# Kernel optimization log

Measured on AMD Instinct MI355X. Metric: run time of the kernel, lower is better.

## Reference

```python
import jax, jax.numpy as jnp
import numpy as np

NUM_GRAPHS = 64


def setup_inputs() -> dict:
    key = jax.random.key(0)
    ks = jax.random.split(key, 8)
    N, E, D_IN, D_H = 50000, 800000, 128, 256
    x = jax.random.uniform(ks[0], (N, D_IN), dtype=jnp.float32)
    edge_index = jax.random.randint(ks[1], (2, E), 0, N, dtype=jnp.int64)
    batch = jnp.sort(jax.random.randint(ks[2], (N,), 0, NUM_GRAPHS, dtype=jnp.int64))
    s = 1.0 / np.sqrt(D_IN)
    s2 = 1.0 / np.sqrt(D_H)
    W1_rel = jax.random.normal(ks[3], (D_IN, D_H), dtype=jnp.float32) * s
    W1_root = jax.random.normal(ks[4], (D_IN, D_H), dtype=jnp.float32) * s
    b1 = jnp.zeros((D_H,), jnp.float32)
    W2_rel = jax.random.normal(ks[5], (D_H, D_H), dtype=jnp.float32) * s2
    W2_root = jax.random.normal(ks[6], (D_H, D_H), dtype=jnp.float32) * s2
    b2 = jnp.zeros((D_H,), jnp.float32)
    return {"x": x, "edge_index": edge_index, "batch": batch,
            "W1_rel": W1_rel, "W1_root": W1_root, "b1": b1,
            "W2_rel": W2_rel, "W2_root": W2_root, "b2": b2}


def reference(x, edge_index, batch, W1_rel, W1_root, b1, W2_rel, W2_root, b2):
    N = x.shape[0]
    src, dst = edge_index[0], edge_index[1]

    # handcrafted features: per-label fraction of total feature mass + log(graph_size)
    graph_size = jnp.sum(x)
    handcrafted = jnp.concatenate([jnp.sum(x, axis=0) / graph_size,
                                   jnp.log(graph_size)[None]])

    def graph_conv(h, W_rel, W_root, b):
        # PyG GraphConv (aggr='add'): out_i = W_rel @ sum_{j->i} h_j + W_root @ h_i + b
        agg = jax.ops.segment_sum(h[src], dst, num_segments=N)  # [N, d]
        return agg @ W_rel + h @ W_root + b

    h = jax.nn.relu(graph_conv(x, W1_rel, W1_root, b1))
    # layers 2..num_layers share the same weights (module instance reused in original)
    for _ in range(2):
        h = jax.nn.relu(graph_conv(h, W2_rel, W2_root, b2))

    # global_mean_pool over batch ids
    counts = jax.ops.segment_sum(jnp.ones((N,), h.dtype), batch, num_segments=NUM_GRAPHS)
    pooled = jax.ops.segment_sum(h, batch, num_segments=NUM_GRAPHS)
    pooled = pooled / jnp.maximum(counts, 1.0)[:, None]
    return pooled, handcrafted
```

## Files before the change

kernel.cpp:

```cpp
#include <hip/hip_runtime.h>
#include <hip/hip_bf16.h>
#include <string.h>

#define NN 50000
#define NE 800000
#define DIN 128
#define DH 256
#define NG 64
#define PSPLIT 32
#define GCAP 2048

typedef short bf16x8 __attribute__((ext_vector_type(8)));
typedef float f32x4 __attribute__((ext_vector_type(4)));
typedef unsigned int u32x2 __attribute__((ext_vector_type(2)));

__device__ __forceinline__ float bf2f(__hip_bfloat16 v) { return __bfloat162float(v); }
__device__ __forceinline__ float bfbits(unsigned int lo16) {
  unsigned int u = lo16 << 16;
  float f;
  memcpy(&f, &u, 4);
  return f;
}
__device__ __forceinline__ unsigned int packbf2(float x, float y) {
  __hip_bfloat16 bx = __float2bfloat16(x), by = __float2bfloat16(y);
  unsigned short ux, uy;
  memcpy(&ux, &bx, 2);
  memcpy(&uy, &by, 2);
  return (unsigned int)ux | ((unsigned int)uy << 16);
}

__device__ __forceinline__ float loadF(const void* p, long i, int fbf) {
  return fbf ? bf2f(((const __hip_bfloat16*)p)[i]) : ((const float*)p)[i];
}
__device__ __forceinline__ void storeF(void* p, long i, float v, int fbf) {
  if (fbf) ((__hip_bfloat16*)p)[i] = __float2bfloat16(v);
  else ((float*)p)[i] = v;
}
__device__ __forceinline__ int loadI(const void* p, long i, int i64) {
  return i64 ? (int)((const long long*)p)[i] : ((const int*)p)[i];
}

__global__ void k_zero_detect(int* __restrict__ p, int n, const void* __restrict__ x,
                              const void* __restrict__ ei, int* __restrict__ flags) {
  int i = blockIdx.x * blockDim.x + threadIdx.x;
  int stride = gridDim.x * blockDim.x;
  for (int k = i; k < n; k += stride) p[k] = 0;
  if (blockIdx.x == 0) {
    __shared__ int s_f32sig, s_i32sig;
    if (threadIdx.x == 0) { s_f32sig = 0; s_i32sig = 0; }
    __syncthreads();
    int t = threadIdx.x;
    const unsigned short* u = (const unsigned short*)x;
    int f = 0;
    for (int j = 2 * t; j < 8192; j += 512) if (u[j] >= 0x4000) f = 1;
    const unsigned int* w = (const unsigned int*)ei;
    int g = 0;
    for (int j = 2 * t + 1; j < 8192; j += 512) if (w[j] != 0u) g = 1;
    if (f) atomicOr(&s_f32sig, 1);
    if (g) atomicOr(&s_i32sig, 1);
    __syncthreads();
    if (t == 0) { flags[0] = s_f32sig ? 0 : 1; flags[1] = s_i32sig ? 0 : 1; }
  }
}

__global__ __launch_bounds__(256) void k_prep(
    const void* __restrict__ x, __hip_bfloat16* __restrict__ xs,
    float* __restrict__ colsum, const int* __restrict__ flags) {
  int fbf = flags[0];
  int t = threadIdx.x;
  int lane16 = t & 15;
  int rowoff = t >> 4;
  float acc[8] = {};
  for (int r = blockIdx.x * 16 + rowoff; r < NN; r += gridDim.x * 16) {
    uint4 o;
    if (fbf) {
      uint4 v = ((const uint4*)x)[(long)r * 16 + lane16];
      acc[0] += bfbits(v.x & 0xffffu); acc[1] += bfbits(v.x >> 16);
      acc[2] += bfbits(v.y & 0xffffu); acc[3] += bfbits(v.y >> 16);
      acc[4] += bfbits(v.z & 0xffffu); acc[5] += bfbits(v.z >> 16);
      acc[6] += bfbits(v.w & 0xffffu); acc[7] += bfbits(v.w >> 16);
      o = v;
    } else {
      float4 a = ((const float4*)x)[(long)r * 32 + lane16 * 2];
      float4 b = ((const float4*)x)[(long)r * 32 + lane16 * 2 + 1];
      acc[0] += a.x; acc[1] += a.y; acc[2] += a.z; acc[3] += a.w;
      acc[4] += b.x; acc[5] += b.y; acc[6] += b.z; acc[7] += b.w;
      o.x = packbf2(a.x, a.y); o.y = packbf2(a.z, a.w);
      o.z = packbf2(b.x, b.y); o.w = packbf2(b.z, b.w);
    }
    ((uint4*)xs)[((long)(lane16 >> 2) * NN + r) * 4 + (lane16 & 3)] = o;
  }
  __shared__ float s[16][DIN];
#pragma unroll
  for (int k = 0; k < 8; ++k) s[rowoff][lane16 * 8 + k] = acc[k];
  __syncthreads();
  if (t < DIN) {
    float v = 0.f;
#pragma unroll
    for (int ro = 0; ro < 16; ++ro) v += s[ro][t];
    atomicAdd(&colsum[t], v);
  }
}

__global__ void k_handcrafted(const float* __restrict__ colsum, void* __restrict__ out,
                              const int* __restrict__ flags) {
  __shared__ float s[DIN];
  int fbf = flags[0];
  int t = threadIdx.x;
  s[t] = colsum[t];
  __syncthreads();
  for (int off = DIN / 2; off > 0; off >>= 1) {
    if (t < off) s[t] += s[t + off];
    __syncthreads();
  }
  float g = s[0];
  storeF(out, NG * DH + t, colsum[t] / g, fbf);
  if (t == 0) storeF(out, NG * DH + DIN, logf(g), fbf);
}

__global__ void k_pack_w(const void* __restrict__ Wrel, const void* __restrict__ Wroot,
                         const void* __restrict__ bias, __hip_bfloat16* __restrict__ pack,
                         float* __restrict__ biasf, const int* __restrict__ flags, int K) {
  int fbf = flags[0];
  int KS = K >> 5;
  int total = 2 * K * DH;
  int i = blockIdx.x * blockDim.x + threadIdx.x;
  int stride = gridDim.x * blockDim.x;
  for (int p = i; p < total; p += stride) {
    int m = p / (K * DH);
    int r = p % (K * DH);
    int j = r & 7;
    int l = (r >> 3) & 63;
    int q2 = r >> 9;
    int ks = q2 % KS;
    int ct = q2 / KS;
    int kk = ks * 32 + (l >> 4) * 8 + j;
    int col = ct * 16 + (l & 15);
    const void* W = m ? Wroot : Wrel;
    pack[p] = __float2bfloat16(loadF(W, (long)kk * DH + col, fbf));
  }
  if (i < DH) biasf[i] = loadF(bias, i, fbf);
}

__global__ void k_deg(const void* __restrict__ ei, int* __restrict__ cnt,
                      const int* __restrict__ flags) {
  int i64 = flags[1];
  int e = blockIdx.x * blockDim.x + threadIdx.x;
  int stride = gridDim.x * blockDim.x;
  for (; e < NE; e += stride) {
    int d = loadI(ei, (long)NE + e, i64);
    d = min(max(d, 0), NN - 1);
    atomicAdd(&cnt[d], 1);
  }
}

#define SCAN_B 256
__global__ void k_scan1(const int* __restrict__ cnt, int* __restrict__ rowptr,
                        int* __restrict__ bsum) {
  __shared__ int s[SCAN_B];
  int b = blockIdx.x, t = threadIdx.x;
  int i = b * SCAN_B + t;
  int v = (i < NN) ? cnt[i] : 0;
  s[t] = v;
  __syncthreads();
  for (int off = 1; off < SCAN_B; off <<= 1) {
    int xv = (t >= off) ? s[t - off] : 0;
    __syncthreads();
    s[t] += xv;
    __syncthreads();
  }
  if (i < NN) rowptr[i] = s[t] - v;
  if (t == SCAN_B - 1) bsum[b] = s[t];
}

__global__ void k_scan2(int* __restrict__ bsum, int nb) {
  __shared__ int s[SCAN_B];
  int t = threadIdx.x;
  int v = (t < nb) ? bsum[t] : 0;
  s[t] = v;
  __syncthreads();
  for (int off = 1; off < SCAN_B; off <<= 1) {
    int xv = (t >= off) ? s[t - off] : 0;
    __syncthreads();
    s[t] += xv;
    __syncthreads();
  }
  if (t < nb) bsum[t] = s[t] - v;
}

__global__ void k_scan3b(int* __restrict__ rowptr, const int* __restrict__ bsum,
                         const void* __restrict__ batch, int* __restrict__ gstart,
                         int* __restrict__ gend, const int* __restrict__ flags) {
  int i64 = flags[1];
  int i = blockIdx.x * blockDim.x + threadIdx.x;
  int stride = gridDim.x * blockDim.x;
  for (; i < NN; i += stride) {
    rowptr[i] += bsum[i >> 8];
    int b = min(max(loadI(batch, i, i64), 0), NG - 1);
    int bp = (i == 0) ? -1 : min(max(loadI(batch, i - 1, i64), 0), NG - 1);
    if (b != bp) gstart[b] = i;
    int bn = (i == NN - 1) ? -1 : min(max(loadI(batch, i + 1, i64), 0), NG - 1);
    if (b != bn) gend[b] = i + 1;
  }
  if (blockIdx.x == 0 && threadIdx.x == 0) rowptr[NN] = NE;
}

__global__ void k_fill(const void* __restrict__ ei, const int* __restrict__ rowptr,
                       int* __restrict__ cur, int* __restrict__ srcs,
                       const int* __restrict__ flags) {
  int i64 = flags[1];
  int e = blockIdx.x * blockDim.x + threadIdx.x;
  int stride = gridDim.x * blockDim.x;
  for (; e < NE; e += stride) {
    int s = loadI(ei, e, i64);
    int d = loadI(ei, (long)NE + e, i64);
    s = min(max(s, 0), NN - 1);
    d = min(max(d, 0), NN - 1);
    int p = atomicAdd(&cur[d], 1);
    srcs[rowptr[d] + p] = s;
  }
}

template <int K>
__global__ __launch_bounds__(256) void k_gathers(
    const int* __restrict__ rowptr, const int* __restrict__ srcs,
    const __hip_bfloat16* __restrict__ hs, __hip_bfloat16* __restrict__ agg) {
  constexpr int SL = K / 32;
  constexpr int HALVES = 8 / SL;
  constexpr int NPH = (NN + HALVES - 1) / HALVES;
  constexpr int NPB = 16;
  __shared__ int se[GCAP];
  __shared__ int sb[2];
  int role = blockIdx.x & 7;
  int nb = blockIdx.x >> 3;
  int s = role / HALVES;
  int half = role % HALVES;
  int t = threadIdx.x;
  int n0 = half * NPH + nb * NPB;
  int nlim = min((half + 1) * NPH, NN);
  if (t == 0) {
    sb[0] = rowptr[min(n0, nlim)];
    sb[1] = rowptr[min(n0 + NPB, nlim)];
  }
  __syncthreads();
  int wbeg = sb[0];
  int wlen = min(sb[1] - wbeg, GCAP);
  for (int i = t; i < wlen; i += 256)
    se[i] = __builtin_nontemporal_load(&srcs[wbeg + i]);
  __syncthreads();
  int nsub = t >> 4;
  int sub = (t >> 3) & 1;
  int c = t & 7;
  int node = n0 + nsub;
  if (node >= nlim) return;
  const u32x2* hb = (const u32x2*)hs + (long)s * NN * 8 + c;
  u32x2* agg2 = (u32x2*)agg;
  int beg = rowptr[node], end = rowptr[node + 1];
  float a0 = 0.f, a1 = 0.f, a2 = 0.f, a3 = 0.f;
  if (end - wbeg <= wlen) {
    int ib = beg - wbeg, ie = end - wbeg;
    for (int i = ib + sub * 8; i < ie; i += 16) {
      int idx[8];
      float m[8];
      u32x2 v[8];
#pragma unroll
      for (int u = 0; u < 8; ++u) {
        int j = i + u;
        int ok = j < ie;
        idx[u] = se[ok ? j : ib];
        m[u] = ok ? 1.f : 0.f;
      }
#pragma unroll
      for (int u = 0; u < 8; ++u) v[u] = hb[(long)idx[u] * 8];
#pragma unroll
      for (int u = 0; u < 8; ++u) {
        a0 = fmaf(m[u], bfbits(v[u].x & 0xffffu), a0);
        a1 = fmaf(m[u], bfbits(v[u].x >> 16), a1);
        a2 = fmaf(m[u], bfbits(v[u].y & 0xffffu), a2);
        a3 = fmaf(m[u], bfbits(v[u].y >> 16), a3);
      }
    }
  } else {
    for (int i = beg + sub * 8; i < end; i += 16) {
      int idx[8];
      float m[8];
      u32x2 v[8];
#pragma unroll
      for (int u = 0; u < 8; ++u) {
        int j = i + u;
        int ok = j < end;
        idx[u] = __builtin_nontemporal_load(&srcs[ok ? j : beg]);
        m[u] = ok ? 1.f : 0.f;
      }
#pragma unroll
      for (int u = 0; u < 8; ++u) v[u] = hb[(long)idx[u] * 8];
#pragma unroll
      for (int u = 0; u < 8; ++u) {
        a0 = fmaf(m[u], bfbits(v[u].x & 0xffffu), a0);
        a1 = fmaf(m[u], bfbits(v[u].x >> 16), a1);
        a2 = fmaf(m[u], bfbits(v[u].y & 0xffffu), a2);
        a3 = fmaf(m[u], bfbits(v[u].y >> 16), a3);
      }
    }
  }
  a0 += __shfl_xor(a0, 8);
  a1 += __shfl_xor(a1, 8);
  a2 += __shfl_xor(a2, 8);
  a3 += __shfl_xor(a3, 8);
  if (sub == 0) {
    u32x2 o;
    o.x = packbf2(a0, a1);
    o.y = packbf2(a2, a3);
    __builtin_nontemporal_store(o, &agg2[(long)node * (K / 4) + s * 8 + c]);
  }
}

template <int K, bool OUTS>
__global__ __launch_bounds__(256, 4) void k_gemm(
    const __hip_bfloat16* __restrict__ A1, const __hip_bfloat16* __restrict__ A2,
    const __hip_bfloat16* __restrict__ Wpack, const float* __restrict__ bias,
    __hip_bfloat16* __restrict__ out) {
  constexpr int KS = K >> 5;
  int lane = threadIdx.x & 63;
  int wave = threadIdx.x >> 6;
  int m15 = lane & 15;
  int q = lane >> 4;
  int row0 = blockIdx.x * 32;
  const short* A1s = (const short*)A1;
  const short* A2s = (const short*)A2;
  const short* Wp = (const short*)Wpack;
  const int wrootOfs = K * DH;
  f32x4 acc[2][4] = {};
#pragma unroll
  for (int ks = 0; ks < KS; ++ks) {
    int kofs = ks * 32 + q * 8;
    bf16x8 a1[2], a2[2], b1[4], b2[4];
#pragma unroll
    for (int mt = 0; mt < 2; ++mt) {
      int r = row0 + mt * 16 + m15;
      if (r > NN - 1) r = NN - 1;
      a1[mt] = *(const bf16x8*)(A1s + (long)r * K + kofs);
      a2[mt] = *(const bf16x8*)(A2s + ((long)ks * NN + r) * 32 + q * 8);
    }
#pragma unroll
    for (int ct = 0; ct < 4; ++ct) {
      int gct = wave * 4 + ct;
      const short* base = Wp + ((gct * KS + ks) * 64 + lane) * 8;
      b1[ct] = *(const bf16x8*)(base);
      b2[ct] = *(const bf16x8*)(base + wrootOfs);
    }
#pragma unroll
    for (int mt = 0; mt < 2; ++mt)
#pragma unroll
      for (int ct = 0; ct < 4; ++ct) {
        acc[mt][ct] = __builtin_amdgcn_mfma_f32_16x16x32_bf16(a1[mt], b1[ct], acc[mt][ct], 0, 0, 0);
        acc[mt][ct] = __builtin_amdgcn_mfma_f32_16x16x32_bf16(a2[mt], b2[ct], acc[mt][ct], 0, 0, 0);
      }
  }
#pragma unroll
  for (int mt = 0; mt < 2; ++mt)
#pragma unroll
    for (int ct = 0; ct < 4; ++ct) {
      int col = (wave * 4 + ct) * 16 + m15;
      float bv = bias[col];
#pragma unroll
      for (int r = 0; r < 4; ++r) {
        int row = row0 + mt * 16 + q * 4 + r;
        if (row < NN) {
          float v = acc[mt][ct][r] + bv;
          long oidx = OUTS ? (((long)(col >> 5) * NN + row) * 32 + (col & 31))
                           : ((long)row * DH + col);
          out[oidx] = __float2bfloat16(fmaxf(v, 0.f));
        }
      }
    }
}

__global__ void k_poolpart(const int* __restrict__ gstart, const int* __restrict__ gend,
                           const __hip_bfloat16* __restrict__ h, float* __restrict__ pooled) {
  int g = blockIdx.x;
  int p = blockIdx.y;
  int j = threadIdx.x;
  int s = gstart[g], e = gend[g];
  int len = e - s;
  if (len <= 0) return;
  int chunk = (len + PSPLIT - 1) / PSPLIT;
  int rs = s + p * chunk;
  int re = min(rs + chunk, e);
  if (rs >= re) return;
  const unsigned int* h2 = (const unsigned int*)h;
  float a0 = 0.f, a1 = 0.f;
  for (int r = rs; r < re; ++r) {
    unsigned int v = h2[(long)r * 128 + j];
    a0 += bfbits(v & 0xffffu);
    a1 += bfbits(v >> 16);
  }
  atomicAdd(&pooled[g * DH + 2 * j], a0);
  atomicAdd(&pooled[g * DH + 2 * j + 1], a1);
}

__global__ void k_poolfin(const int* __restrict__ gstart, const int* __restrict__ gend,
                          const float* __restrict__ pooled, void* __restrict__ out,
                          const int* __restrict__ flags) {
  int fbf = flags[0];
  int g = blockIdx.x;
  int j = threadIdx.x;
  float cnt = fmaxf((float)(gend[g] - gstart[g]), 1.0f);
  storeF(out, (long)g * DH + j, pooled[g * DH + j] / cnt, fbf);
}

extern "C" void kernel_launch(void* const* d_in, const int* in_sizes, int n_in,
                              void* d_out, int out_size, void* d_ws, size_t ws_size,
                              hipStream_t stream) {
  const void* x = d_in[0];
  const void* ei = d_in[1];
  const void* batch = d_in[2];
  const void* W1r = d_in[3];
  const void* W1o = d_in[4];
  const void* b1 = d_in[5];
  const void* W2r = d_in[6];
  const void* W2o = d_in[7];
  const void* b2 = d_in[8];
  void* out = d_out;

  char* w = (char*)d_ws;
  auto alloc = [&](size_t bytes) -> char* {
    char* p = w;
    w += (bytes + 255) & ~(size_t)255;
    return p;
  };
  int* flags = (int*)alloc(64);
  const int zero_n = NN + NN + DIN + NG + NG + NG * DH;
  int* zreg = (int*)alloc((size_t)zero_n * 4);
  int* cnt = zreg;
  int* cur = cnt + NN;
  float* colsum = (float*)(cur + NN);
  int* gstart = (int*)(colsum + DIN);
  int* gend = gstart + NG;
  float* pooled = (float*)(gend + NG);
  int* rowptr = (int*)alloc((NN + 1) * 4);
  int* bsum = (int*)alloc(SCAN_B * 4);
  int* srcs = (int*)alloc((size_t)NE * 4);
  __hip_bfloat16* xs = (__hip_bfloat16*)alloc((size_t)NN * DIN * 2);
  __hip_bfloat16* aggb = (__hip_bfloat16*)alloc((size_t)NN * DH * 2);
  __hip_bfloat16* h1s = (__hip_bfloat16*)alloc((size_t)NN * DH * 2);
  __hip_bfloat16* h2s = (__hip_bfloat16*)alloc((size_t)NN * DH * 2);
  __hip_bfloat16* wp1 = (__hip_bfloat16*)alloc((size_t)2 * DIN * DH * 2);
  __hip_bfloat16* wp2 = (__hip_bfloat16*)alloc((size_t)2 * DH * DH * 2);
  float* b1f = (float*)alloc(DH * 4);
  float* b2f = (float*)alloc(DH * 4);
  __hip_bfloat16* hA = h1s;

  const int nblk = (NN + SCAN_B - 1) / SCAN_B;
  const int gemm_grid = (NN + 31) / 32;
  const int g256_grid = 8 * ((NN + 15) / 16);
  const int g128_grid = 8 * ((NN / 2 + 15) / 16);

  k_zero_detect<<<512, 256, 0, stream>>>(zreg, zero_n, x, ei, flags);

  k_pack_w<<<64, 256, 0, stream>>>(W1r, W1o, b1, wp1, b1f, flags, DIN);
  k_pack_w<<<128, 256, 0, stream>>>(W2r, W2o, b2, wp2, b2f, flags, DH);
  k_prep<<<1024, 256, 0, stream>>>(x, xs, colsum, flags);
  k_handcrafted<<<1, 128, 0, stream>>>(colsum, out, flags);

  k_deg<<<1024, 256, 0, stream>>>(ei, cnt, flags);
  k_scan1<<<nblk, SCAN_B, 0, stream>>>(cnt, rowptr, bsum);
  k_scan2<<<1, SCAN_B, 0, stream>>>(bsum, nblk);
  k_scan3b<<<256, 256, 0, stream>>>(rowptr, bsum, batch, gstart, gend, flags);
  k_fill<<<1024, 256, 0, stream>>>(ei, rowptr, cur, srcs, flags);

  k_gathers<DIN><<<g128_grid, 256, 0, stream>>>(rowptr, srcs, xs, aggb);
  k_gemm<DIN, true><<<gemm_grid, 256, 0, stream>>>(aggb, xs, wp1, b1f, h1s);
  k_gathers<DH><<<g256_grid, 256, 0, stream>>>(rowptr, srcs, h1s, aggb);
  k_gemm<DH, true><<<gemm_grid, 256, 0, stream>>>(aggb, h1s, wp2, b2f, h2s);
  k_gathers<DH><<<g256_grid, 256, 0, stream>>>(rowptr, srcs, h2s, aggb);
  k_gemm<DH, false><<<gemm_grid, 256, 0, stream>>>(aggb, h2s, wp2, b2f, hA);

  k_poolpart<<<dim3(NG, PSPLIT), 128, 0, stream>>>(gstart, gend, hA, pooled);
  k_poolfin<<<NG, DH, 0, stream>>>(gstart, gend, pooled, out, flags);
}
```

Baseline: 532.5 us.

## Balance gather work by splitting block edge ranges evenly across thread groups

Rewrites the CSR gather kernel so each block covers 32 nodes and splits its whole edge range evenly among 32 thread groups, instead of giving each node's edges to a fixed 16-thread group. Each edge is tagged with its local node via a binary search over row pointers, and partial sums are flushed into a shared-memory accumulator with LDS atomics whenever the node changes. This targets load imbalance from varying node degrees and raises per-thread memory-level parallelism with 16 loads in flight. In exchange it adds LDS atomics, a per-edge binary search, and padded shared accumulators.

```diff
diff --git a/kernel.cpp b/kernel.cpp
--- a/kernel.cpp
+++ b/kernel.cpp
@@ -8,7 +8,7 @@
 #define DH 256
 #define NG 64
 #define PSPLIT 32
-#define GCAP 2048
+#define GCAP 1024
 
 typedef short bf16x8 __attribute__((ext_vector_type(8)));
 typedef float f32x4 __attribute__((ext_vector_type(4)));
@@ -228,9 +228,10 @@
   constexpr int SL = K / 32;
   constexpr int HALVES = 8 / SL;
   constexpr int NPH = (NN + HALVES - 1) / HALVES;
-  constexpr int NPB = 16;
-  __shared__ int se[GCAP];
-  __shared__ int sb[2];
+  constexpr int NPB = 32;
+  __shared__ int srow[NPB + 1];
+  __shared__ unsigned int se[GCAP];
+  __shared__ float sacc[NPB * 33];
   int role = blockIdx.x & 7;
   int nb = blockIdx.x >> 3;
   int s = role / HALVES;
@@ -238,80 +239,79 @@
   int t = threadIdx.x;
   int n0 = half * NPH + nb * NPB;
   int nlim = min((half + 1) * NPH, NN);
-  if (t == 0) {
-    sb[0] = rowptr[min(n0, nlim)];
-    sb[1] = rowptr[min(n0 + NPB, nlim)];
-  }
+  if (n0 >= nlim) return;
+  if (t <= NPB) srow[t] = rowptr[min(n0 + t, nlim)];
+  for (int i = t; i < NPB * 33; i += 256) sacc[i] = 0.f;
   __syncthreads();
-  int wbeg = sb[0];
-  int wlen = min(sb[1] - wbeg, GCAP);
-  for (int i = t; i < wlen; i += 256)
-    se[i] = __builtin_nontemporal_load(&srcs[wbeg + i]);
-  __syncthreads();
-  int nsub = t >> 4;
-  int sub = (t >> 3) & 1;
+  int wbeg = srow[0];
+  int wtot = srow[NPB] - wbeg;
+  int g = t >> 3;
   int c = t & 7;
-  int node = n0 + nsub;
-  if (node >= nlim) return;
   const u32x2* hb = (const u32x2*)hs + (long)s * NN * 8 + c;
-  u32x2* agg2 = (u32x2*)agg;
-  int beg = rowptr[node], end = rowptr[node + 1];
-  float a0 = 0.f, a1 = 0.f, a2 = 0.f, a3 = 0.f;
-  if (end - wbeg <= wlen) {
-    int ib = beg - wbeg, ie = end - wbeg;
-    for (int i = ib + sub * 8; i < ie; i += 16) {
-      int idx[8];
-      float m[8];
-      u32x2 v[8];
-#pragma unroll
-      for (int u = 0; u < 8; ++u) {
-        int j = i + u;
-        int ok = j < ie;
-        idx[u] = se[ok ? j : ib];
-        m[u] = ok ? 1.f : 0.f;
+  for (int wo = 0; wo < wtot; wo += GCAP) {
+    int seglen = min(GCAP, wtot - wo);
+    for (int i = t; i < seglen; i += 256) {
+      int eabs = wbeg + wo + i;
+      int sv = __builtin_nontemporal_load(&srcs[eabs]);
+      int lo = 0;
+#pragma unroll
+      for (int st = 16; st >= 1; st >>= 1)
+        if (srow[lo + st] <= eabs) lo += st;
+      se[i] = (unsigned)sv | ((unsigned)lo << 20);
+    }
+    __syncthreads();
+    int chunk = (seglen + NPB - 1) / NPB;
+    int ib = g * chunk;
+    int ie = min(ib + chunk, seglen);
+    if (ib < ie) {
+      int cur = (int)(se[ib] >> 20);
+      float a0 = 0.f, a1 = 0.f, a2 = 0.f, a3 = 0.f;
+      for (int i0 = ib; i0 < ie; i0 += 16) {
+        unsigned pk[16];
+        u32x2 v[16];
+#pragma unroll
+        for (int u = 0; u < 16; ++u) {
+          int j = i0 + u;
+          unsigned p = se[j < ie ? j : ie - 1];
+          pk[u] = p;
+          v[u] = hb[(long)(p & 0xFFFFFu) * 8];
+        }
+#pragma unroll
+        for (int u = 0; u < 16; ++u) {
+          int nn = (int)(pk[u] >> 20);
+          if (nn != cur) {
+            atomicAdd(&sacc[cur * 33 + c * 4 + 0], a0);
+            atomicAdd(&sacc[cur * 33 + c * 4 + 1], a1);
+            atomicAdd(&sacc[cur * 33 + c * 4 + 2], a2);
+            atomicAdd(&sacc[cur * 33 + c * 4 + 3], a3);
+            a0 = a1 = a2 = a3 = 0.f;
+            cur = nn;
+          }
+          float m = (i0 + u < ie) ? 1.f : 0.f;
+          a0 = fmaf(m, bfbits(v[u].x & 0xffffu), a0);
+          a1 = fmaf(m, bfbits(v[u].x >> 16), a1);
+          a2 = fmaf(m, bfbits(v[u].y & 0xffffu), a2);
+          a3 = fmaf(m, bfbits(v[u].y >> 16), a3);
+        }
       }
-#pragma unroll
-      for (int u = 0; u < 8; ++u) v[u] = hb[(long)idx[u] * 8];
-#pragma unroll
-      for (int u = 0; u < 8; ++u) {
-        a0 = fmaf(m[u], bfbits(v[u].x & 0xffffu), a0);
-        a1 = fmaf(m[u], bfbits(v[u].x >> 16), a1);
-        a2 = fmaf(m[u], bfbits(v[u].y & 0xffffu), a2);
-        a3 = fmaf(m[u], bfbits(v[u].y >> 16), a3);
-      }
-    }
-  } else {
-    for (int i = beg + sub * 8; i < end; i += 16) {
-      int idx[8];
-      float m[8];
-      u32x2 v[8];
-#pragma unroll
-      for (int u = 0; u < 8; ++u) {
-        int j = i + u;
-        int ok = j < end;
-        idx[u] = __builtin_nontemporal_load(&srcs[ok ? j : beg]);
-        m[u] = ok ? 1.f : 0.f;
-      }
-#pragma unroll
-      for (int u = 0; u < 8; ++u) v[u] = hb[(long)idx[u] * 8];
-#pragma unroll
-      for (int u = 0; u < 8; ++u) {
-        a0 = fmaf(m[u], bfbits(v[u].x & 0xffffu), a0);
-        a1 = fmaf(m[u], bfbits(v[u].x >> 16), a1);
-        a2 = fmaf(m[u], bfbits(v[u].y & 0xffffu), a2);
-        a3 = fmaf(m[u], bfbits(v[u].y >> 16), a3);
-      }
-    }
-  }
-  a0 += __shfl_xor(a0, 8);
-  a1 += __shfl_xor(a1, 8);
-  a2 += __shfl_xor(a2, 8);
-  a3 += __shfl_xor(a3, 8);
-  if (sub == 0) {
+      atomicAdd(&sacc[cur * 33 + c * 4 + 0], a0);
+      atomicAdd(&sacc[cur * 33 + c * 4 + 1], a1);
+      atomicAdd(&sacc[cur * 33 + c * 4 + 2], a2);
+      atomicAdd(&sacc[cur * 33 + c * 4 + 3], a3);
+    }
+    __syncthreads();
+  }
+  int en = t >> 3;
+  int node = n0 + en;
+  if (node < nlim) {
+    float b0 = sacc[en * 33 + c * 4 + 0];
+    float b1 = sacc[en * 33 + c * 4 + 1];
+    float b2 = sacc[en * 33 + c * 4 + 2];
+    float b3 = sacc[en * 33 + c * 4 + 3];
     u32x2 o;
-    o.x = packbf2(a0, a1);
-    o.y = packbf2(a2, a3);
-    __builtin_nontemporal_store(o, &agg2[(long)node * (K / 4) + s * 8 + c]);
+    o.x = packbf2(b0, b1);
+    o.y = packbf2(b2, b3);
+    __builtin_nontemporal_store(o, &((u32x2*)agg)[(long)node * (K / 4) + s * 8 + c]);
   }
 }
 
@@ -453,8 +453,8 @@
 
   const int nblk = (NN + SCAN_B - 1) / SCAN_B;
   const int gemm_grid = (NN + 31) / 32;
-  const int g256_grid = 8 * ((NN + 15) / 16);
-  const int g128_grid = 8 * ((NN / 2 + 15) / 16);
+  const int g256_grid = 8 * ((NN + 31) / 32);
+  const int g128_grid = 8 * ((NN / 2 + 31) / 32);
 
   k_zero_detect<<<512, 256, 0, stream>>>(zreg, zero_n, x, ei, flags);
 
```

New measurement: 742.3 us. 1.39x slower.

## Relabel nodes by in-degree to balance gather work per block

Applied to the files above, without the earlier changes.

Computes a degree histogram and counting-sort permutation so nodes are renumbered in order of in-degree, rewrites CSR, features and source indices in permuted order, and un-permutes only in the final GEMM store. With similar-degree nodes grouped, the gather kernel drops its two-way edge split and shuffle reduction, using one 8-thread group per node and 32 nodes per block. The aim is to cut warp divergence and load imbalance in the gathers. The cost is extra preprocessing kernels, a single-block histogram scan, and scattered, uncoalesced writes in k_prep and the last GEMM.

```diff
diff --git a/kernel.cpp b/kernel.cpp
--- a/kernel.cpp
+++ b/kernel.cpp
@@ -9,6 +9,7 @@
 #define NG 64
 #define PSPLIT 32
 #define GCAP 2048
+#define NBIN 1024
 
 typedef short bf16x8 __attribute__((ext_vector_type(8)));
 typedef float f32x4 __attribute__((ext_vector_type(4)));
@@ -63,9 +64,54 @@
   }
 }
 
+__global__ void k_deg(const void* __restrict__ ei, int* __restrict__ cnt,
+                      const int* __restrict__ flags) {
+  int i64 = flags[1];
+  int e = blockIdx.x * blockDim.x + threadIdx.x;
+  int stride = gridDim.x * blockDim.x;
+  for (; e < NE; e += stride) {
+    int d = loadI(ei, (long)NE + e, i64);
+    d = min(max(d, 0), NN - 1);
+    atomicAdd(&cnt[d], 1);
+  }
+}
+
+__global__ __launch_bounds__(NBIN) void k_histscan(const int* __restrict__ cnt,
+                                                   int* __restrict__ hist,
+                                                   int* __restrict__ histbase) {
+  __shared__ int lh[NBIN];
+  int t = threadIdx.x;
+  lh[t] = 0;
+  __syncthreads();
+  for (int o = t; o < NN; o += NBIN) atomicAdd(&lh[min(cnt[o], NBIN - 1)], 1);
+  __syncthreads();
+  int v = lh[t];
+  for (int off = 1; off < NBIN; off <<= 1) {
+    int xv = (t >= off) ? lh[t - off] : 0;
+    __syncthreads();
+    lh[t] += xv;
+    __syncthreads();
+  }
+  histbase[t] = lh[t] - v;
+  (void)hist;
+}
+
+__global__ void k_perm(const int* __restrict__ cnt, int* __restrict__ histbase,
+                       int* __restrict__ perm, int* __restrict__ inv) {
+  int o = blockIdx.x * blockDim.x + threadIdx.x;
+  int stride = gridDim.x * blockDim.x;
+  for (; o < NN; o += stride) {
+    int bin = min(cnt[o], NBIN - 1);
+    int p = atomicAdd(&histbase[bin], 1);
+    perm[p] = o;
+    inv[o] = p;
+  }
+}
+
 __global__ __launch_bounds__(256) void k_prep(
     const void* __restrict__ x, __hip_bfloat16* __restrict__ xs,
-    float* __restrict__ colsum, const int* __restrict__ flags) {
+    float* __restrict__ colsum, const int* __restrict__ flags,
+    const int* __restrict__ inv) {
   int fbf = flags[0];
   int t = threadIdx.x;
   int lane16 = t & 15;
@@ -88,7 +134,8 @@
       o.x = packbf2(a.x, a.y); o.y = packbf2(a.z, a.w);
       o.z = packbf2(b.x, b.y); o.w = packbf2(b.z, b.w);
     }
-    ((uint4*)xs)[((long)(lane16 >> 2) * NN + r) * 4 + (lane16 & 3)] = o;
+    int pi = inv[r];
+    ((uint4*)xs)[((long)(lane16 >> 2) * NN + pi) * 4 + (lane16 & 3)] = o;
   }
   __shared__ float s[16][DIN];
 #pragma unroll
@@ -142,25 +189,13 @@
   if (i < DH) biasf[i] = loadF(bias, i, fbf);
 }
 
-__global__ void k_deg(const void* __restrict__ ei, int* __restrict__ cnt,
-                      const int* __restrict__ flags) {
-  int i64 = flags[1];
-  int e = blockIdx.x * blockDim.x + threadIdx.x;
-  int stride = gridDim.x * blockDim.x;
-  for (; e < NE; e += stride) {
-    int d = loadI(ei, (long)NE + e, i64);
-    d = min(max(d, 0), NN - 1);
-    atomicAdd(&cnt[d], 1);
-  }
-}
-
 #define SCAN_B 256
-__global__ void k_scan1(const int* __restrict__ cnt, int* __restrict__ rowptr,
-                        int* __restrict__ bsum) {
+__global__ void k_scan1(const int* __restrict__ cnt, const int* __restrict__ perm,
+                        int* __restrict__ rowptr, int* __restrict__ bsum) {
   __shared__ int s[SCAN_B];
   int b = blockIdx.x, t = threadIdx.x;
   int i = b * SCAN_B + t;
-  int v = (i < NN) ? cnt[i] : 0;
+  int v = (i < NN) ? cnt[perm[i]] : 0;
   s[t] = v;
   __syncthreads();
   for (int off = 1; off < SCAN_B; off <<= 1) {
@@ -207,15 +242,15 @@
 
 __global__ void k_fill(const void* __restrict__ ei, const int* __restrict__ rowptr,
                        int* __restrict__ cur, int* __restrict__ srcs,
-                       const int* __restrict__ flags) {
+                       const int* __restrict__ inv, const int* __restrict__ flags) {
   int i64 = flags[1];
   int e = blockIdx.x * blockDim.x + threadIdx.x;
   int stride = gridDim.x * blockDim.x;
   for (; e < NE; e += stride) {
     int s = loadI(ei, e, i64);
     int d = loadI(ei, (long)NE + e, i64);
-    s = min(max(s, 0), NN - 1);
-    d = min(max(d, 0), NN - 1);
+    s = inv[min(max(s, 0), NN - 1)];
+    d = inv[min(max(d, 0), NN - 1)];
     int p = atomicAdd(&cur[d], 1);
     srcs[rowptr[d] + p] = s;
   }
@@ -228,7 +263,6 @@
   constexpr int SL = K / 32;
   constexpr int HALVES = 8 / SL;
   constexpr int NPH = (NN + HALVES - 1) / HALVES;
-  constexpr int NPB = 16;
   __shared__ int se[GCAP];
   __shared__ int sb[2];
   int role = blockIdx.x & 7;
@@ -236,11 +270,12 @@
   int s = role / HALVES;
   int half = role % HALVES;
   int t = threadIdx.x;
-  int n0 = half * NPH + nb * NPB;
+  int n0 = half * NPH + nb * 32;
   int nlim = min((half + 1) * NPH, NN);
+  if (n0 >= nlim) return;
   if (t == 0) {
-    sb[0] = rowptr[min(n0, nlim)];
-    sb[1] = rowptr[min(n0 + NPB, nlim)];
+    sb[0] = rowptr[n0];
+    sb[1] = rowptr[min(n0 + 32, nlim)];
   }
   __syncthreads();
   int wbeg = sb[0];
@@ -248,8 +283,7 @@
   for (int i = t; i < wlen; i += 256)
     se[i] = __builtin_nontemporal_load(&srcs[wbeg + i]);
   __syncthreads();
-  int nsub = t >> 4;
-  int sub = (t >> 3) & 1;
+  int nsub = t >> 3;
   int c = t & 7;
   int node = n0 + nsub;
   if (node >= nlim) return;
@@ -259,7 +293,7 @@
   float a0 = 0.f, a1 = 0.f, a2 = 0.f, a3 = 0.f;
   if (end - wbeg <= wlen) {
     int ib = beg - wbeg, ie = end - wbeg;
-    for (int i = ib + sub * 8; i < ie; i += 16) {
+    for (int i = ib; i < ie; i += 8) {
       int idx[8];
       float m[8];
       u32x2 v[8];
@@ -281,7 +315,7 @@
       }
     }
   } else {
-    for (int i = beg + sub * 8; i < end; i += 16) {
+    for (int i = beg; i < end; i += 8) {
       int idx[8];
       float m[8];
       u32x2 v[8];
@@ -303,23 +337,17 @@
       }
     }
   }
-  a0 += __shfl_xor(a0, 8);
-  a1 += __shfl_xor(a1, 8);
-  a2 += __shfl_xor(a2, 8);
-  a3 += __shfl_xor(a3, 8);
-  if (sub == 0) {
-    u32x2 o;
-    o.x = packbf2(a0, a1);
-    o.y = packbf2(a2, a3);
-    __builtin_nontemporal_store(o, &agg2[(long)node * (K / 4) + s * 8 + c]);
-  }
+  u32x2 o;
+  o.x = packbf2(a0, a1);
+  o.y = packbf2(a2, a3);
+  __builtin_nontemporal_store(o, &agg2[(long)node * (K / 4) + s * 8 + c]);
 }
 
 template <int K, bool OUTS>
 __global__ __launch_bounds__(256, 4) void k_gemm(
     const __hip_bfloat16* __restrict__ A1, const __hip_bfloat16* __restrict__ A2,
     const __hip_bfloat16* __restrict__ Wpack, const float* __restrict__ bias,
-    __hip_bfloat16* __restrict__ out) {
+    __hip_bfloat16* __restrict__ out, const int* __restrict__ perm) {
   constexpr int KS = K >> 5;
   int lane = threadIdx.x & 63;
   int wave = threadIdx.x >> 6;
@@ -358,7 +386,13 @@
       }
   }
 #pragma unroll
-  for (int mt = 0; mt < 2; ++mt)
+  for (int mt = 0; mt < 2; ++mt) {
+    int prow[4];
+#pragma unroll
+    for (int r = 0; r < 4; ++r) {
+      int row = row0 + mt * 16 + q * 4 + r;
+      prow[r] = (!OUTS && row < NN) ? perm[row] : row;
+    }
 #pragma unroll
     for (int ct = 0; ct < 4; ++ct) {
       int col = (wave * 4 + ct) * 16 + m15;
@@ -369,11 +403,12 @@
         if (row < NN) {
           float v = acc[mt][ct][r] + bv;
           long oidx = OUTS ? (((long)(col >> 5) * NN + row) * 32 + (col & 31))
-                           : ((long)row * DH + col);
+                           : ((long)prow[r] * DH + col);
           out[oidx] = __float2bfloat16(fmaxf(v, 0.f));
         }
       }
     }
+  }
 }
 
 __global__ void k_poolpart(const int* __restrict__ gstart, const int* __restrict__ gend,
@@ -430,14 +465,18 @@
     return p;
   };
   int* flags = (int*)alloc(64);
-  const int zero_n = NN + NN + DIN + NG + NG + NG * DH;
+  const int zero_n = NBIN + NN + NN + DIN + NG + NG + NG * DH;
   int* zreg = (int*)alloc((size_t)zero_n * 4);
-  int* cnt = zreg;
+  int* hist = zreg;
+  int* cnt = hist + NBIN;
   int* cur = cnt + NN;
   float* colsum = (float*)(cur + NN);
   int* gstart = (int*)(colsum + DIN);
   int* gend = gstart + NG;
   float* pooled = (float*)(gend + NG);
+  int* histbase = (int*)alloc(NBIN * 4);
+  int* perm = (int*)alloc(NN * 4);
+  int* inv = (int*)alloc(NN * 4);
   int* rowptr = (int*)alloc((NN + 1) * 4);
   int* bsum = (int*)alloc(SCAN_B * 4);
   int* srcs = (int*)alloc((size_t)NE * 4);
@@ -453,28 +492,32 @@
 
   const int nblk = (NN + SCAN_B - 1) / SCAN_B;
   const int gemm_grid = (NN + 31) / 32;
-  const int g256_grid = 8 * ((NN + 15) / 16);
-  const int g128_grid = 8 * ((NN / 2 + 15) / 16);
+  const int g256_grid = 8 * ((NN + 31) / 32);
+  const int g128_grid = 8 * ((NN / 2 + 31) / 32);
 
   k_zero_detect<<<512, 256, 0, stream>>>(zreg, zero_n, x, ei, flags);
 
   k_pack_w<<<64, 256, 0, stream>>>(W1r, W1o, b1, wp1, b1f, flags, DIN);
   k_pack_w<<<128, 256, 0, stream>>>(W2r, W2o, b2, wp2, b2f, flags, DH);
-  k_prep<<<1024, 256, 0, stream>>>(x, xs, colsum, flags);
+
+  k_deg<<<1024, 256, 0, stream>>>(ei, cnt, flags);
+  k_histscan<<<1, NBIN, 0, stream>>>(cnt, hist, histbase);
+  k_perm<<<256, 256, 0, stream>>>(cnt, histbase, perm, inv);
+
+  k_prep<<<1024, 256, 0, stream>>>(x, xs, colsum, flags, inv);
   k_handcrafted<<<1, 128, 0, stream>>>(colsum, out, flags);
 
-  k_deg<<<1024, 256, 0, stream>>>(ei, cnt, flags);
-  k_scan1<<<nblk, SCAN_B, 0, stream>>>(cnt, rowptr, bsum);
+  k_scan1<<<nblk, SCAN_B, 0, stream>>>(cnt, perm, rowptr, bsum);
   k_scan2<<<1, SCAN_B, 0, stream>>>(bsum, nblk);
   k_scan3b<<<256, 256, 0, stream>>>(rowptr, bsum, batch, gstart, gend, flags);
-  k_fill<<<1024, 256, 0, stream>>>(ei, rowptr, cur, srcs, flags);
+  k_fill<<<1024, 256, 0, stream>>>(ei, rowptr, cur, srcs, inv, flags);
 
   k_gathers<DIN><<<g128_grid, 256, 0, stream>>>(rowptr, srcs, xs, aggb);
-  k_gemm<DIN, true><<<gemm_grid, 256, 0, stream>>>(aggb, xs, wp1, b1f, h1s);
+  k_gemm<DIN, true><<<gemm_grid, 256, 0, stream>>>(aggb, xs, wp1, b1f, h1s, perm);
   k_gathers<DH><<<g256_grid, 256, 0, stream>>>(rowptr, srcs, h1s, aggb);
-  k_gemm<DH, true><<<gemm_grid, 256, 0, stream>>>(aggb, h1s, wp2, b2f, h2s);
+  k_gemm<DH, true><<<gemm_grid, 256, 0, stream>>>(aggb, h1s, wp2, b2f, h2s, perm);
   k_gathers<DH><<<g256_grid, 256, 0, stream>>>(rowptr, srcs, h2s, aggb);
-  k_gemm<DH, false><<<gemm_grid, 256, 0, stream>>>(aggb, h2s, wp2, b2f, hA);
+  k_gemm<DH, false><<<gemm_grid, 256, 0, stream>>>(aggb, h2s, wp2, b2f, hA, perm);
 
   k_poolpart<<<dim3(NG, PSPLIT), 128, 0, stream>>>(gstart, gend, hA, pooled);
   k_poolfin<<<NG, DH, 0, stream>>>(gstart, gend, pooled, out, flags);
```

New measurement: 654.5 us. 1.23x slower.
